# Kernel optimization log

Measured on AMD Instinct MI355X. Metric: run time of the kernel, lower is better.

The kernel has to match this reference:

```python
import jax, jax.numpy as jnp
import numpy as np
import math

N_HEAD = 16
N_KV_HEAD = 4
N_EMBD = 2048
HEAD_DIM = N_EMBD // N_HEAD  # 128
SCALE = 1.0 / math.sqrt(HEAD_DIM)
B, T = 2, 2048


def setup_inputs() -> dict:
    key = jax.random.key(0)
    ks = jax.random.split(key, 5)
    s = 0.02
    x = jax.random.normal(ks[0], (B, T, N_EMBD), dtype=jnp.float32)
    wq = jax.random.normal(ks[1], (N_EMBD, N_EMBD), dtype=jnp.float32) * s
    wk = jax.random.normal(ks[2], (N_KV_HEAD * HEAD_DIM, N_EMBD), dtype=jnp.float32) * s
    wv = jax.random.normal(ks[3], (N_KV_HEAD * HEAD_DIM, N_EMBD), dtype=jnp.float32) * s
    wo = jax.random.normal(ks[4], (N_EMBD, N_EMBD), dtype=jnp.float32) * s
    return {"x": x, "wq": wq, "wk": wk, "wv": wv, "wo": wo}


def _forward(x, wq, wk, wv, wo):
    b, t, _ = x.shape
    # Linear layers: y = x @ W.T  (torch Linear weight is (out,in))
    q = (x @ wq.T).reshape(b, t, N_HEAD, HEAD_DIM).transpose(0, 2, 1, 3)      # (B,H,T,D)
    k = (x @ wk.T).reshape(b, t, N_KV_HEAD, HEAD_DIM).transpose(0, 2, 1, 3)  # (B,Hkv,T,D)
    v = (x @ wv.T).reshape(b, t, N_KV_HEAD, HEAD_DIM).transpose(0, 2, 1, 3)
    groups = N_HEAD // N_KV_HEAD
    k = jnp.repeat(k, groups, axis=1)  # repeat_interleave over head dim -> (B,H,T,D)
    v = jnp.repeat(v, groups, axis=1)
    # Causal mask: True above diagonal (masked-out positions)
    mask = jnp.triu(jnp.ones((t, t), dtype=bool), k=1)[None, None]  # (1,1,T,T)
    scores = jnp.einsum('bhqd,bhkd->bhqk', q, k) * SCALE
    scores = jnp.where(mask, -jnp.inf, scores)
    attn = jax.nn.softmax(scores, axis=-1)
    attn = jnp.where(mask, 0.0, attn)
    y = jnp.einsum('bhqk,bhkd->bhqd', attn, v)       # (B,H,T,D)
    y = y.transpose(0, 2, 1, 3).reshape(b, t, N_EMBD)
    return y @ wo.T


def reference(x, wq, wk, wv, wo):
    return _forward(x, wq, wk, wv, wo)
```

## Files before the change

### kernel.cpp

```cpp
#include <hip/hip_runtime.h>
#include <cstdint>
#include <cstddef>

typedef __bf16 bf16_t;
typedef __bf16 bf16x8 __attribute__((ext_vector_type(8)));
typedef __bf16 bf16x4 __attribute__((ext_vector_type(4)));
typedef float f32x4 __attribute__((ext_vector_type(4)));

#define GL2LDS16(gptr, lptr)                                                   \
  __builtin_amdgcn_global_load_lds(                                            \
      (__attribute__((address_space(1))) void*)(gptr),                         \
      (__attribute__((address_space(3))) void*)(lptr), 16, 0, 0)

__device__ __forceinline__ float fast_exp2(float x) {
  float r;
  asm volatile("v_exp_f32 %0, %1" : "=v"(r) : "v"(x));
  return r;
}

#define BATCH 2
#define T_SEQ 2048
#define NH 16
#define NKV 4
#define HD 128
#define EMB 2048
#define KVDIM (NKV * HD)
#define MROWS (BATCH * T_SEQ)

__global__ void cvt_all(const float4* __restrict__ x,  const float4* __restrict__ wq,
                        const float4* __restrict__ wk, const float4* __restrict__ wv,
                        const float4* __restrict__ wo,
                        bf16x4* __restrict__ xb,  bf16x4* __restrict__ wqb,
                        bf16x4* __restrict__ wkb, bf16x4* __restrict__ wvb,
                        bf16x4* __restrict__ wob) {
  const int blk = blockIdx.x;
  const float4* src;
  bf16x4* dst;
  int base;
  if (blk < 8192)       { src = x;  dst = xb;  base = blk; }
  else if (blk < 12288) { src = wq; dst = wqb; base = blk - 8192; }
  else if (blk < 13312) { src = wk; dst = wkb; base = blk - 12288; }
  else if (blk < 14336) { src = wv; dst = wvb; base = blk - 13312; }
  else                  { src = wo; dst = wob; base = blk - 14336; }
  const int i = base * 256 + threadIdx.x;
  const float4 v = src[i];
  dst[i] = bf16x4{(__bf16)v.x, (__bf16)v.y, (__bf16)v.z, (__bf16)v.w};
}

__global__ __launch_bounds__(256, 2)
void gemm_qkv(const bf16_t* __restrict__ A,
              const bf16_t* __restrict__ Wq, const bf16_t* __restrict__ Wk,
              const bf16_t* __restrict__ Wv,
              bf16_t* __restrict__ Qb, bf16_t* __restrict__ Kb,
              bf16_t* __restrict__ Vt, float qalpha)
{
  __shared__ bf16_t As[128 * 64];
  __shared__ bf16_t Bs[128 * 64];

  const int tid  = threadIdx.x;
  const int lane = tid & 63;
  const int wv   = tid >> 6;
  const int nbx = blockIdx.x;
  const int m0 = blockIdx.y * 128;
  const int wm = (wv >> 1) * 64;
  const int wn = (wv & 1) * 64;
  const int l15 = lane & 15;
  const int lq  = lane >> 4;

  const bf16_t* Bm;
  int ncol0;
  if (nbx < 16)      { Bm = Wq; ncol0 = nbx * 128; }
  else if (nbx < 20) { Bm = Wk; ncol0 = (nbx - 16) * 128; }
  else               { Bm = Wv; ncol0 = (nbx - 20) * 128; }

  f32x4 acc[4][4] = {};

  const int srow = tid >> 3;
  const int scol = (tid & 7) * 8;

  for (int k0 = 0; k0 < EMB; k0 += 64) {
#pragma unroll
    for (int r = 0; r < 4; ++r) {
      const int row = r * 32 + srow;
      GL2LDS16(A + (size_t)(m0 + row) * EMB + k0 + scol, As + row * 64 + scol);
    }
#pragma unroll
    for (int r = 0; r < 4; ++r) {
      const int row = r * 32 + srow;
      GL2LDS16(Bm + (size_t)(ncol0 + row) * EMB + k0 + scol, Bs + row * 64 + scol);
    }
    __syncthreads();

#pragma unroll
    for (int ks = 0; ks < 2; ++ks) {
      const int kc = ks * 32 + lq * 8;
      bf16x8 af[4], bf[4];
#pragma unroll
      for (int i = 0; i < 4; ++i)
        af[i] = *(const bf16x8*)(As + (wm + i * 16 + l15) * 64 + kc);
#pragma unroll
      for (int j = 0; j < 4; ++j)
        bf[j] = *(const bf16x8*)(Bs + (wn + j * 16 + l15) * 64 + kc);
#pragma unroll
      for (int i = 0; i < 4; ++i)
#pragma unroll
        for (int j = 0; j < 4; ++j)
          acc[i][j] = __builtin_amdgcn_mfma_f32_16x16x32_bf16(af[i], bf[j], acc[i][j], 0, 0, 0);
    }
    __syncthreads();
  }

  if (nbx < 16) {
#pragma unroll
    for (int i = 0; i < 4; ++i) {
      const int rbase = m0 + wm + i * 16 + lq * 4;
#pragma unroll
      for (int j = 0; j < 4; ++j) {
        const int col = ncol0 + wn + j * 16 + l15;
#pragma unroll
        for (int r = 0; r < 4; ++r)
          Qb[(size_t)(rbase + r) * EMB + col] = (bf16_t)(acc[i][j][r] * qalpha);
      }
    }
  } else if (nbx < 20) {
#pragma unroll
    for (int i = 0; i < 4; ++i) {
      const int rbase = m0 + wm + i * 16 + lq * 4;
#pragma unroll
      for (int j = 0; j < 4; ++j) {
        const int col = ncol0 + wn + j * 16 + l15;
#pragma unroll
        for (int r = 0; r < 4; ++r)
          Kb[(size_t)(rbase + r) * KVDIM + col] = (bf16_t)acc[i][j][r];
      }
    }
  } else {
    const int b = m0 >> 11;
    const int mloc0 = (m0 & 2047) + wm + lq * 4;
#pragma unroll
    for (int i = 0; i < 4; ++i) {
      const int mloc = mloc0 + i * 16;
#pragma unroll
      for (int j = 0; j < 4; ++j) {
        const int d = ncol0 + wn + j * 16 + l15;
        *(bf16x4*)(Vt + (size_t)(b * KVDIM + d) * T_SEQ + mloc) =
            bf16x4{(__bf16)acc[i][j][0], (__bf16)acc[i][j][1],
                   (__bf16)acc[i][j][2], (__bf16)acc[i][j][3]};
      }
    }
  }
}

__global__ __launch_bounds__(256, 2)
void gemm_out(const bf16_t* __restrict__ A, const bf16_t* __restrict__ Bm,
              float* __restrict__ C, int M, int N, int K)
{
  __shared__ bf16_t As[128 * 64];
  __shared__ bf16_t Bs[128 * 64];

  const int tid  = threadIdx.x;
  const int lane = tid & 63;
  const int wv   = tid >> 6;
  const int m0 = blockIdx.y * 128;
  const int n0 = blockIdx.x * 128;
  const int wm = (wv >> 1) * 64;
  const int wn = (wv & 1) * 64;
  const int l15 = lane & 15;
  const int lq  = lane >> 4;

  f32x4 acc[4][4] = {};
  const int srow = tid >> 3;
  const int scol = (tid & 7) * 8;

  for (int k0 = 0; k0 < K; k0 += 64) {
#pragma unroll
    for (int r = 0; r < 4; ++r) {
      const int row = r * 32 + srow;
      GL2LDS16(A + (size_t)(m0 + row) * K + k0 + scol, As + row * 64 + scol);
    }
#pragma unroll
    for (int r = 0; r < 4; ++r) {
      const int row = r * 32 + srow;
      GL2LDS16(Bm + (size_t)(n0 + row) * K + k0 + scol, Bs + row * 64 + scol);
    }
    __syncthreads();

#pragma unroll
    for (int ks = 0; ks < 2; ++ks) {
      const int kc = ks * 32 + lq * 8;
      bf16x8 af[4], bf[4];
#pragma unroll
      for (int i = 0; i < 4; ++i)
        af[i] = *(const bf16x8*)(As + (wm + i * 16 + l15) * 64 + kc);
#pragma unroll
      for (int j = 0; j < 4; ++j)
        bf[j] = *(const bf16x8*)(Bs + (wn + j * 16 + l15) * 64 + kc);
#pragma unroll
      for (int i = 0; i < 4; ++i)
#pragma unroll
        for (int j = 0; j < 4; ++j)
          acc[i][j] = __builtin_amdgcn_mfma_f32_16x16x32_bf16(af[i], bf[j], acc[i][j], 0, 0, 0);
    }
    __syncthreads();
  }

#pragma unroll
  for (int i = 0; i < 4; ++i) {
    const int rbase = m0 + wm + i * 16 + lq * 4;
#pragma unroll
    for (int j = 0; j < 4; ++j) {
      const int col = n0 + wn + j * 16 + l15;
#pragma unroll
      for (int r = 0; r < 4; ++r)
        C[(size_t)(rbase + r) * N + col] = acc[i][j][r];
    }
  }
}

__global__ __launch_bounds__(256)
void attn_fwd(const bf16_t* __restrict__ Q, const bf16_t* __restrict__ Kg,
              const bf16_t* __restrict__ Vt, bf16_t* __restrict__ Y)
{
  __shared__ bf16_t Ks[2][64 * 128];
  __shared__ bf16_t Vs[128 * 64];
  __shared__ bf16_t Ps[2][4][16 * 64];

  const int tid  = threadIdx.x;
  const int lane = tid & 63;
  const int wv   = tid >> 6;
  const int l15  = lane & 15;
  const int lq   = lane >> 4;
  const int h  = blockIdx.y;
  const int b  = blockIdx.z;
  const int hkv = h >> 2;
  const int q7 = l15 & 7;
  bf16_t* P0 = Ps[0][wv];
  bf16_t* P1 = Ps[1][wv];

  auto stageK = [&](int kt, int bufsel) {
    const int base_t = b * T_SEQ + kt * 64;
#pragma unroll
    for (int r = 0; r < 4; ++r) {
      const int c = r * 256 + tid;
      const int row = c >> 4, p = c & 15;
      const int sb = p ^ (row & 7);
      GL2LDS16(Kg + (size_t)(base_t + row) * KVDIM + hkv * HD + sb * 8,
               &Ks[bufsel][c * 8]);
    }
  };
  auto stageV = [&](int kt) {
#pragma unroll
    for (int r = 0; r < 4; ++r) {
      const int c = r * 256 + tid;
      const int row = c >> 3, p = c & 7;
      const int sb = p ^ (row & 7);
      GL2LDS16(Vt + (size_t)(b * KVDIM + hkv * HD + row) * T_SEQ + kt * 64 + sb * 8,
               &Vs[c * 8]);
    }
  };

#pragma unroll 1
  for (int ph = 0; ph < 2; ++ph) {
    const int qt = ph ? blockIdx.x : (15 - blockIdx.x);
    const int q0 = qt * 128;
    const int nkt = 2 * qt + 2;
    const int qa0 = q0 + wv * 16 + l15;
    const int qa1 = qa0 + 64;

    bf16x8 qf0[4], qf1[4];
    {
      const bf16_t* qp0 = Q + ((size_t)(b * T_SEQ + qa0) * NH + h) * HD + lq * 8;
      const bf16_t* qp1 = Q + ((size_t)(b * T_SEQ + qa1) * NH + h) * HD + lq * 8;
#pragma unroll
      for (int ds = 0; ds < 4; ++ds) {
        qf0[ds] = *(const bf16x8*)(qp0 + ds * 32);
        qf1[ds] = *(const bf16x8*)(qp1 + ds * 32);
      }
    }

    float l0 = 0.f, l1 = 0.f;
    f32x4 o0[8], o1[8];
#pragma unroll
    for (int nb = 0; nb < 8; ++nb) {
      o0[nb] = f32x4{0.f, 0.f, 0.f, 0.f};
      o1[nb] = f32x4{0.f, 0.f, 0.f, 0.f};
    }

    __syncthreads();
    stageK(0, 0);

    for (int kt = 0; kt < nkt; ++kt) {
      const int cur = kt & 1;
      __syncthreads();
      stageV(kt);
      if (kt + 1 < nkt) stageK(kt + 1, cur ^ 1);

      const bool g0 = (kt < nkt - 1);

      f32x4 s0[4], s1[4];
#pragma unroll
      for (int nb = 0; nb < 4; ++nb) {
        s0[nb] = f32x4{0.f, 0.f, 0.f, 0.f};
        s1[nb] = f32x4{0.f, 0.f, 0.f, 0.f};
        const int row = nb * 16 + l15;
        const int r7  = row & 7;
#pragma unroll
        for (int ds = 0; ds < 4; ++ds) {
          const bf16x8 kf = *(const bf16x8*)&Ks[cur][row * 128 + (((ds * 4 + lq) ^ r7) * 8)];
          if (g0) s0[nb] = __builtin_amdgcn_mfma_f32_16x16x32_bf16(kf, qf0[ds], s0[nb], 0, 0, 0);
          s1[nb] = __builtin_amdgcn_mfma_f32_16x16x32_bf16(kf, qf1[ds], s1[nb], 0, 0, 0);
        }
      }

      if (g0) {
        const bool dia = (kt == nkt - 2);
#pragma unroll
        for (int nb = 0; nb < 4; ++nb) {
          const int kvb = kt * 64 + nb * 16 + lq * 4;
          float p0, p1, p2, p3;
          if (dia) {
            p0 = (kvb + 0 <= qa0) ? fast_exp2(s0[nb][0]) : 0.f;
            p1 = (kvb + 1 <= qa0) ? fast_exp2(s0[nb][1]) : 0.f;
            p2 = (kvb + 2 <= qa0) ? fast_exp2(s0[nb][2]) : 0.f;
            p3 = (kvb + 3 <= qa0) ? fast_exp2(s0[nb][3]) : 0.f;
          } else {
            p0 = fast_exp2(s0[nb][0]); p1 = fast_exp2(s0[nb][1]);
            p2 = fast_exp2(s0[nb][2]); p3 = fast_exp2(s0[nb][3]);
          }
          l0 += (p0 + p1) + (p2 + p3);
          *(bf16x4*)(P0 + l15 * 64 + (((nb * 4 + lq) ^ q7) << 2)) =
              bf16x4{(__bf16)p0, (__bf16)p1, (__bf16)p2, (__bf16)p3};
        }
      }
      {
        const bool dia = (kt == nkt - 1);
#pragma unroll
        for (int nb = 0; nb < 4; ++nb) {
          const int kvb = kt * 64 + nb * 16 + lq * 4;
          float p0, p1, p2, p3;
          if (dia) {
            p0 = (kvb + 0 <= qa1) ? fast_exp2(s1[nb][0]) : 0.f;
            p1 = (kvb + 1 <= qa1) ? fast_exp2(s1[nb][1]) : 0.f;
            p2 = (kvb + 2 <= qa1) ? fast_exp2(s1[nb][2]) : 0.f;
            p3 = (kvb + 3 <= qa1) ? fast_exp2(s1[nb][3]) : 0.f;
          } else {
            p0 = fast_exp2(s1[nb][0]); p1 = fast_exp2(s1[nb][1]);
            p2 = fast_exp2(s1[nb][2]); p3 = fast_exp2(s1[nb][3]);
          }
          l1 += (p0 + p1) + (p2 + p3);
          *(bf16x4*)(P1 + l15 * 64 + (((nb * 4 + lq) ^ q7) << 2)) =
              bf16x4{(__bf16)p0, (__bf16)p1, (__bf16)p2, (__bf16)p3};
        }
      }

      __syncthreads();
      asm volatile("s_waitcnt lgkmcnt(0)" ::: "memory");

#pragma unroll
      for (int ks = 0; ks < 2; ++ks) {
        const int blA = ((ks * 8 + 2 * lq) ^ q7) << 2;
        const int blB = ((ks * 8 + 2 * lq + 1) ^ q7) << 2;
        const bf16x4 a0 = *(const bf16x4*)(P0 + l15 * 64 + blA);
        const bf16x4 b0 = *(const bf16x4*)(P0 + l15 * 64 + blB);
        const bf16x4 a1 = *(const bf16x4*)(P1 + l15 * 64 + blA);
        const bf16x4 b1 = *(const bf16x4*)(P1 + l15 * 64 + blB);
        const bf16x8 pf0 = __builtin_shufflevector(a0, b0, 0, 1, 2, 3, 4, 5, 6, 7);
        const bf16x8 pf1 = __builtin_shufflevector(a1, b1, 0, 1, 2, 3, 4, 5, 6, 7);
#pragma unroll
        for (int nb = 0; nb < 8; ++nb) {
          const int row = nb * 16 + l15;
          const bf16x8 vf = *(const bf16x8*)&Vs[row * 64 + (((ks * 4 + lq) ^ (row & 7)) * 8)];
          if (g0) o0[nb] = __builtin_amdgcn_mfma_f32_16x16x32_bf16(vf, pf0, o0[nb], 0, 0, 0);
          o1[nb] = __builtin_amdgcn_mfma_f32_16x16x32_bf16(vf, pf1, o1[nb], 0, 0, 0);
        }
      }
    }

    {
      float lt = l0;
      lt += __shfl_xor(lt, 16);
      lt += __shfl_xor(lt, 32);
      const float inv = 1.f / lt;
      bf16_t* yp = Y + ((size_t)(b * T_SEQ + qa0) * NH + h) * HD + lq * 4;
#pragma unroll
      for (int nb = 0; nb < 8; ++nb)
        *(bf16x4*)(yp + nb * 16) = bf16x4{(__bf16)(o0[nb][0] * inv), (__bf16)(o0[nb][1] * inv),
                                          (__bf16)(o0[nb][2] * inv), (__bf16)(o0[nb][3] * inv)};
    }
    {
      float lt = l1;
      lt += __shfl_xor(lt, 16);
      lt += __shfl_xor(lt, 32);
      const float inv = 1.f / lt;
      bf16_t* yp = Y + ((size_t)(b * T_SEQ + qa1) * NH + h) * HD + lq * 4;
#pragma unroll
      for (int nb = 0; nb < 8; ++nb)
        *(bf16x4*)(yp + nb * 16) = bf16x4{(__bf16)(o1[nb][0] * inv), (__bf16)(o1[nb][1] * inv),
                                          (__bf16)(o1[nb][2] * inv), (__bf16)(o1[nb][3] * inv)};
    }
  }
}

extern "C" void kernel_launch(void* const* d_in, const int* in_sizes, int n_in,
                              void* d_out, int out_size, void* d_ws, size_t ws_size,
                              hipStream_t stream) {
  const float* x  = (const float*)d_in[0];
  const float* wq = (const float*)d_in[1];
  const float* wk = (const float*)d_in[2];
  const float* wv = (const float*)d_in[3];
  const float* wo = (const float*)d_in[4];
  float* out = (float*)d_out;

  const size_t n_x  = (size_t)MROWS * EMB;
  const size_t n_wq = (size_t)EMB * EMB;
  const size_t n_wk = (size_t)KVDIM * EMB;

  bf16_t* xb  = (bf16_t*)d_ws;
  bf16_t* wqb = xb  + n_x;
  bf16_t* wkb = wqb + n_wq;
  bf16_t* wvb = wkb + n_wk;
  bf16_t* wob = wvb + n_wk;
  bf16_t* Qb  = wob + n_wq;
  bf16_t* Kb  = Qb + (size_t)MROWS * EMB;
  bf16_t* Vtb = Kb + (size_t)MROWS * KVDIM;
  bf16_t* Yb  = Vtb + (size_t)MROWS * KVDIM;

  dim3 blk(256);

  cvt_all<<<dim3(18432), blk, 0, stream>>>(
      (const float4*)x, (const float4*)wq, (const float4*)wk, (const float4*)wv, (const float4*)wo,
      (bf16x4*)xb, (bf16x4*)wqb, (bf16x4*)wkb, (bf16x4*)wvb, (bf16x4*)wob);

  const float qalpha = 0.08838834764831845f * 1.4426950408889634f;
  gemm_qkv<<<dim3(24, MROWS / 128), blk, 0, stream>>>(xb, wqb, wkb, wvb,
                                                      Qb, Kb, Vtb, qalpha);

  attn_fwd<<<dim3(8, NH, BATCH), blk, 0, stream>>>(Qb, Kb, Vtb, Yb);

  gemm_out<<<dim3(EMB / 128, MROWS / 128), blk, 0, stream>>>(Yb, wob, out, MROWS, EMB, EMB);
}
```

Before: 337.6 us.

## Keep P in registers via 16x16x16 MFMA, double-buffer V, one tile per block

The attention kernel stops staging the probability tile P through shared memory. The PV product now uses the 16x16x16 bf16 MFMA, whose operand layout matches the score accumulator output, so P can be fed straight from registers. V is double-buffered and prefetched together with the next K tile, which removes the second barrier per iteration. The grid doubles to one query tile per block with launch_bounds(256,2) instead of two paired tiles per block, which loses the causal load balancing the pairing gave in exchange for more blocks and occupancy.

```diff
diff --git a/kernel.cpp b/kernel.cpp
--- a/kernel.cpp
+++ b/kernel.cpp
@@ -5,6 +5,7 @@
 typedef __bf16 bf16_t;
 typedef __bf16 bf16x8 __attribute__((ext_vector_type(8)));
 typedef __bf16 bf16x4 __attribute__((ext_vector_type(4)));
+typedef short s16x4 __attribute__((ext_vector_type(4)));
 typedef float f32x4 __attribute__((ext_vector_type(4)));
 
 #define GL2LDS16(gptr, lptr)                                                   \
@@ -16,6 +17,18 @@
   float r;
   asm volatile("v_exp_f32 %0, %1" : "=v"(r) : "v"(x));
   return r;
+}
+
+__device__ __forceinline__ f32x4 mfma16(bf16x4 a, bf16x4 b, f32x4 c) {
+#if __has_builtin(__builtin_amdgcn_mfma_f32_16x16x16bf16_1k)
+  return __builtin_amdgcn_mfma_f32_16x16x16bf16_1k(
+      __builtin_bit_cast(s16x4, a), __builtin_bit_cast(s16x4, b), c, 0, 0, 0);
+#else
+  f32x4 d = c;
+  asm volatile("v_mfma_f32_16x16x16_bf16 %0, %1, %2, %0"
+               : "+v"(d) : "v"(a), "v"(b));
+  return d;
+#endif
 }
 
 #define BATCH 2
@@ -74,7 +87,6 @@
   else               { Bm = Wv; ncol0 = (nbx - 20) * 128; }
 
   f32x4 acc[4][4] = {};
-
   const int srow = tid >> 3;
   const int scol = (tid & 7) * 8;
 
@@ -217,25 +229,28 @@
   }
 }
 
-__global__ __launch_bounds__(256)
+__global__ __launch_bounds__(256, 2)
 void attn_fwd(const bf16_t* __restrict__ Q, const bf16_t* __restrict__ Kg,
               const bf16_t* __restrict__ Vt, bf16_t* __restrict__ Y)
 {
   __shared__ bf16_t Ks[2][64 * 128];
-  __shared__ bf16_t Vs[128 * 64];
-  __shared__ bf16_t Ps[2][4][16 * 64];
+  __shared__ bf16_t Vs[2][128 * 64];
 
   const int tid  = threadIdx.x;
   const int lane = tid & 63;
   const int wv   = tid >> 6;
   const int l15  = lane & 15;
   const int lq   = lane >> 4;
+  const int q7   = l15 & 7;
   const int h  = blockIdx.y;
   const int b  = blockIdx.z;
   const int hkv = h >> 2;
-  const int q7 = l15 & 7;
-  bf16_t* P0 = Ps[0][wv];
-  bf16_t* P1 = Ps[1][wv];
+
+  const int qt = 15 - blockIdx.x;
+  const int q0 = qt * 128;
+  const int nkt = 2 * qt + 2;
+  const int qa0 = q0 + wv * 16 + l15;
+  const int qa1 = qa0 + 64;
 
   auto stageK = [&](int kt, int bufsel) {
     const int base_t = b * T_SEQ + kt * 64;
@@ -248,156 +263,135 @@
                &Ks[bufsel][c * 8]);
     }
   };
-  auto stageV = [&](int kt) {
+  auto stageV = [&](int kt, int bufsel) {
 #pragma unroll
     for (int r = 0; r < 4; ++r) {
       const int c = r * 256 + tid;
       const int row = c >> 3, p = c & 7;
       const int sb = p ^ (row & 7);
       GL2LDS16(Vt + (size_t)(b * KVDIM + hkv * HD + row) * T_SEQ + kt * 64 + sb * 8,
-               &Vs[c * 8]);
+               &Vs[bufsel][c * 8]);
     }
   };
 
-#pragma unroll 1
-  for (int ph = 0; ph < 2; ++ph) {
-    const int qt = ph ? blockIdx.x : (15 - blockIdx.x);
-    const int q0 = qt * 128;
-    const int nkt = 2 * qt + 2;
-    const int qa0 = q0 + wv * 16 + l15;
-    const int qa1 = qa0 + 64;
-
-    bf16x8 qf0[4], qf1[4];
+  bf16x8 qf0[4], qf1[4];
+  {
+    const bf16_t* qp0 = Q + ((size_t)(b * T_SEQ + qa0) * NH + h) * HD + lq * 8;
+    const bf16_t* qp1 = Q + ((size_t)(b * T_SEQ + qa1) * NH + h) * HD + lq * 8;
+#pragma unroll
+    for (int ds = 0; ds < 4; ++ds) {
+      qf0[ds] = *(const bf16x8*)(qp0 + ds * 32);
+      qf1[ds] = *(const bf16x8*)(qp1 + ds * 32);
+    }
+  }
+
+  float l0 = 0.f, l1 = 0.f;
+  f32x4 o0[8], o1[8];
+#pragma unroll
+  for (int nb = 0; nb < 8; ++nb) {
+    o0[nb] = f32x4{0.f, 0.f, 0.f, 0.f};
+    o1[nb] = f32x4{0.f, 0.f, 0.f, 0.f};
+  }
+
+  stageK(0, 0);
+  stageV(0, 0);
+
+  for (int kt = 0; kt < nkt; ++kt) {
+    const int cur = kt & 1;
+    __syncthreads();
+    if (kt + 1 < nkt) { stageK(kt + 1, cur ^ 1); stageV(kt + 1, cur ^ 1); }
+
+    const bool g0 = (kt < nkt - 1);
+
+    f32x4 s0[4], s1[4];
+#pragma unroll
+    for (int nb = 0; nb < 4; ++nb) {
+      s0[nb] = f32x4{0.f, 0.f, 0.f, 0.f};
+      s1[nb] = f32x4{0.f, 0.f, 0.f, 0.f};
+      const int row = nb * 16 + l15;
+      const int r7  = row & 7;
+#pragma unroll
+      for (int ds = 0; ds < 4; ++ds) {
+        const bf16x8 kf = *(const bf16x8*)&Ks[cur][row * 128 + (((ds * 4 + lq) ^ r7) * 8)];
+        if (g0) s0[nb] = __builtin_amdgcn_mfma_f32_16x16x32_bf16(kf, qf0[ds], s0[nb], 0, 0, 0);
+        s1[nb] = __builtin_amdgcn_mfma_f32_16x16x32_bf16(kf, qf1[ds], s1[nb], 0, 0, 0);
+      }
+    }
+
+    bf16x4 pf0[4], pf1[4];
+    if (g0) {
+      const bool dia = (kt == nkt - 2);
+#pragma unroll
+      for (int nb = 0; nb < 4; ++nb) {
+        const int kvb = kt * 64 + nb * 16 + lq * 4;
+        float p0, p1, p2, p3;
+        if (dia) {
+          p0 = (kvb + 0 <= qa0) ? fast_exp2(s0[nb][0]) : 0.f;
+          p1 = (kvb + 1 <= qa0) ? fast_exp2(s0[nb][1]) : 0.f;
+          p2 = (kvb + 2 <= qa0) ? fast_exp2(s0[nb][2]) : 0.f;
+          p3 = (kvb + 3 <= qa0) ? fast_exp2(s0[nb][3]) : 0.f;
+        } else {
+          p0 = fast_exp2(s0[nb][0]); p1 = fast_exp2(s0[nb][1]);
+          p2 = fast_exp2(s0[nb][2]); p3 = fast_exp2(s0[nb][3]);
+        }
+        l0 += (p0 + p1) + (p2 + p3);
+        pf0[nb] = bf16x4{(__bf16)p0, (__bf16)p1, (__bf16)p2, (__bf16)p3};
+      }
+    }
     {
-      const bf16_t* qp0 = Q + ((size_t)(b * T_SEQ + qa0) * NH + h) * HD + lq * 8;
-      const bf16_t* qp1 = Q + ((size_t)(b * T_SEQ + qa1) * NH + h) * HD + lq * 8;
-#pragma unroll
-      for (int ds = 0; ds < 4; ++ds) {
-        qf0[ds] = *(const bf16x8*)(qp0 + ds * 32);
-        qf1[ds] = *(const bf16x8*)(qp1 + ds * 32);
-      }
-    }
-
-    float l0 = 0.f, l1 = 0.f;
-    f32x4 o0[8], o1[8];
-#pragma unroll
-    for (int nb = 0; nb < 8; ++nb) {
-      o0[nb] = f32x4{0.f, 0.f, 0.f, 0.f};
-      o1[nb] = f32x4{0.f, 0.f, 0.f, 0.f};
-    }
-
-    __syncthreads();
-    stageK(0, 0);
-
-    for (int kt = 0; kt < nkt; ++kt) {
-      const int cur = kt & 1;
-      __syncthreads();
-      stageV(kt);
-      if (kt + 1 < nkt) stageK(kt + 1, cur ^ 1);
-
-      const bool g0 = (kt < nkt - 1);
-
-      f32x4 s0[4], s1[4];
+      const bool dia = (kt == nkt - 1);
 #pragma unroll
       for (int nb = 0; nb < 4; ++nb) {
-        s0[nb] = f32x4{0.f, 0.f, 0.f, 0.f};
-        s1[nb] = f32x4{0.f, 0.f, 0.f, 0.f};
-        const int row = nb * 16 + l15;
-        const int r7  = row & 7;
-#pragma unroll
-        for (int ds = 0; ds < 4; ++ds) {
-          const bf16x8 kf = *(const bf16x8*)&Ks[cur][row * 128 + (((ds * 4 + lq) ^ r7) * 8)];
-          if (g0) s0[nb] = __builtin_amdgcn_mfma_f32_16x16x32_bf16(kf, qf0[ds], s0[nb], 0, 0, 0);
-          s1[nb] = __builtin_amdgcn_mfma_f32_16x16x32_bf16(kf, qf1[ds], s1[nb], 0, 0, 0);
+        const int kvb = kt * 64 + nb * 16 + lq * 4;
+        float p0, p1, p2, p3;
+        if (dia) {
+          p0 = (kvb + 0 <= qa1) ? fast_exp2(s1[nb][0]) : 0.f;
+          p1 = (kvb + 1 <= qa1) ? fast_exp2(s1[nb][1]) : 0.f;
+          p2 = (kvb + 2 <= qa1) ? fast_exp2(s1[nb][2]) : 0.f;
+          p3 = (kvb + 3 <= qa1) ? fast_exp2(s1[nb][3]) : 0.f;
+        } else {
+          p0 = fast_exp2(s1[nb][0]); p1 = fast_exp2(s1[nb][1]);
+          p2 = fast_exp2(s1[nb][2]); p3 = fast_exp2(s1[nb][3]);
         }
-      }
-
-      if (g0) {
-        const bool dia = (kt == nkt - 2);
-#pragma unroll
-        for (int nb = 0; nb < 4; ++nb) {
-          const int kvb = kt * 64 + nb * 16 + lq * 4;
-          float p0, p1, p2, p3;
-          if (dia) {
-            p0 = (kvb + 0 <= qa0) ? fast_exp2(s0[nb][0]) : 0.f;
-            p1 = (kvb + 1 <= qa0) ? fast_exp2(s0[nb][1]) : 0.f;
-            p2 = (kvb + 2 <= qa0) ? fast_exp2(s0[nb][2]) : 0.f;
-            p3 = (kvb + 3 <= qa0) ? fast_exp2(s0[nb][3]) : 0.f;
-          } else {
-            p0 = fast_exp2(s0[nb][0]); p1 = fast_exp2(s0[nb][1]);
-            p2 = fast_exp2(s0[nb][2]); p3 = fast_exp2(s0[nb][3]);
-          }
-          l0 += (p0 + p1) + (p2 + p3);
-          *(bf16x4*)(P0 + l15 * 64 + (((nb * 4 + lq) ^ q7) << 2)) =
-              bf16x4{(__bf16)p0, (__bf16)p1, (__bf16)p2, (__bf16)p3};
-        }
-      }
-      {
-        const bool dia = (kt == nkt - 1);
-#pragma unroll
-        for (int nb = 0; nb < 4; ++nb) {
-          const int kvb = kt * 64 + nb * 16 + lq * 4;
-          float p0, p1, p2, p3;
-          if (dia) {
-            p0 = (kvb + 0 <= qa1) ? fast_exp2(s1[nb][0]) : 0.f;
-            p1 = (kvb + 1 <= qa1) ? fast_exp2(s1[nb][1]) : 0.f;
-            p2 = (kvb + 2 <= qa1) ? fast_exp2(s1[nb][2]) : 0.f;
-            p3 = (kvb + 3 <= qa1) ? fast_exp2(s1[nb][3]) : 0.f;
-          } else {
-            p0 = fast_exp2(s1[nb][0]); p1 = fast_exp2(s1[nb][1]);
-            p2 = fast_exp2(s1[nb][2]); p3 = fast_exp2(s1[nb][3]);
-          }
-          l1 += (p0 + p1) + (p2 + p3);
-          *(bf16x4*)(P1 + l15 * 64 + (((nb * 4 + lq) ^ q7) << 2)) =
-              bf16x4{(__bf16)p0, (__bf16)p1, (__bf16)p2, (__bf16)p3};
-        }
-      }
-
-      __syncthreads();
-      asm volatile("s_waitcnt lgkmcnt(0)" ::: "memory");
-
-#pragma unroll
-      for (int ks = 0; ks < 2; ++ks) {
-        const int blA = ((ks * 8 + 2 * lq) ^ q7) << 2;
-        const int blB = ((ks * 8 + 2 * lq + 1) ^ q7) << 2;
-        const bf16x4 a0 = *(const bf16x4*)(P0 + l15 * 64 + blA);
-        const bf16x4 b0 = *(const bf16x4*)(P0 + l15 * 64 + blB);
-        const bf16x4 a1 = *(const bf16x4*)(P1 + l15 * 64 + blA);
-        const bf16x4 b1 = *(const bf16x4*)(P1 + l15 * 64 + blB);
-        const bf16x8 pf0 = __builtin_shufflevector(a0, b0, 0, 1, 2, 3, 4, 5, 6, 7);
-        const bf16x8 pf1 = __builtin_shufflevector(a1, b1, 0, 1, 2, 3, 4, 5, 6, 7);
-#pragma unroll
-        for (int nb = 0; nb < 8; ++nb) {
-          const int row = nb * 16 + l15;
-          const bf16x8 vf = *(const bf16x8*)&Vs[row * 64 + (((ks * 4 + lq) ^ (row & 7)) * 8)];
-          if (g0) o0[nb] = __builtin_amdgcn_mfma_f32_16x16x32_bf16(vf, pf0, o0[nb], 0, 0, 0);
-          o1[nb] = __builtin_amdgcn_mfma_f32_16x16x32_bf16(vf, pf1, o1[nb], 0, 0, 0);
-        }
-      }
-    }
-
-    {
-      float lt = l0;
-      lt += __shfl_xor(lt, 16);
-      lt += __shfl_xor(lt, 32);
-      const float inv = 1.f / lt;
-      bf16_t* yp = Y + ((size_t)(b * T_SEQ + qa0) * NH + h) * HD + lq * 4;
-#pragma unroll
-      for (int nb = 0; nb < 8; ++nb)
-        *(bf16x4*)(yp + nb * 16) = bf16x4{(__bf16)(o0[nb][0] * inv), (__bf16)(o0[nb][1] * inv),
-                                          (__bf16)(o0[nb][2] * inv), (__bf16)(o0[nb][3] * inv)};
-    }
-    {
-      float lt = l1;
-      lt += __shfl_xor(lt, 16);
-      lt += __shfl_xor(lt, 32);
-      const float inv = 1.f / lt;
-      bf16_t* yp = Y + ((size_t)(b * T_SEQ + qa1) * NH + h) * HD + lq * 4;
-#pragma unroll
-      for (int nb = 0; nb < 8; ++nb)
-        *(bf16x4*)(yp + nb * 16) = bf16x4{(__bf16)(o1[nb][0] * inv), (__bf16)(o1[nb][1] * inv),
-                                          (__bf16)(o1[nb][2] * inv), (__bf16)(o1[nb][3] * inv)};
-    }
+        l1 += (p0 + p1) + (p2 + p3);
+        pf1[nb] = bf16x4{(__bf16)p0, (__bf16)p1, (__bf16)p2, (__bf16)p3};
+      }
+    }
+
+#pragma unroll
+    for (int dt = 0; dt < 8; ++dt) {
+      const int row = dt * 16 + l15;
+#pragma unroll
+      for (int nb = 0; nb < 4; ++nb) {
+        const bf16x4 vf = *(const bf16x4*)&Vs[cur][row * 64 +
+            ((((nb << 1) | (lq >> 1)) ^ q7) << 3) + ((lq & 1) << 2)];
+        if (g0) o0[dt] = mfma16(vf, pf0[nb], o0[dt]);
+        o1[dt] = mfma16(vf, pf1[nb], o1[dt]);
+      }
+    }
+  }
+
+  {
+    float lt = l0;
+    lt += __shfl_xor(lt, 16);
+    lt += __shfl_xor(lt, 32);
+    const float inv = 1.f / lt;
+    bf16_t* yp = Y + ((size_t)(b * T_SEQ + qa0) * NH + h) * HD + lq * 4;
+#pragma unroll
+    for (int nb = 0; nb < 8; ++nb)
+      *(bf16x4*)(yp + nb * 16) = bf16x4{(__bf16)(o0[nb][0] * inv), (__bf16)(o0[nb][1] * inv),
+                                        (__bf16)(o0[nb][2] * inv), (__bf16)(o0[nb][3] * inv)};
+  }
+  {
+    float lt = l1;
+    lt += __shfl_xor(lt, 16);
+    lt += __shfl_xor(lt, 32);
+    const float inv = 1.f / lt;
+    bf16_t* yp = Y + ((size_t)(b * T_SEQ + qa1) * NH + h) * HD + lq * 4;
+#pragma unroll
+    for (int nb = 0; nb < 8; ++nb)
+      *(bf16x4*)(yp + nb * 16) = bf16x4{(__bf16)(o1[nb][0] * inv), (__bf16)(o1[nb][1] * inv),
+                                        (__bf16)(o1[nb][2] * inv), (__bf16)(o1[nb][3] * inv)};
   }
 }
 
@@ -435,7 +429,7 @@
   gemm_qkv<<<dim3(24, MROWS / 128), blk, 0, stream>>>(xb, wqb, wkb, wvb,
                                                       Qb, Kb, Vtb, qalpha);
 
-  attn_fwd<<<dim3(8, NH, BATCH), blk, 0, stream>>>(Qb, Kb, Vtb, Yb);
+  attn_fwd<<<dim3(16, NH, BATCH), blk, 0, stream>>>(Qb, Kb, Vtb, Yb);
 
   gemm_out<<<dim3(EMB / 128, MROWS / 128), blk, 0, stream>>>(Yb, wob, out, MROWS, EMB, EMB);
 }
```

Result: slower. 505.0 us (+49.6%).
